# Performance work log

Measured on AMD Instinct MI355X. Metric: run time of the kernel, lower is better.

## Reference

```python
import jax, jax.numpy as jnp
import numpy as np

N_NODES = 4096
N_EDGES = 500000
N_PAIRS = 2000000
EDGE_DIM = 16
MAX_PATH = 5


def setup_inputs() -> dict:
    key = jax.random.key(0)
    k1, k2, k3, k4, k5 = jax.random.split(key, 5)
    x = jax.random.normal(k1, (N_NODES, EDGE_DIM), dtype=jnp.float32)
    edge_attr = jax.random.normal(k2, (N_EDGES, EDGE_DIM), dtype=jnp.float32)
    path_idx = jax.random.randint(k3, (N_PAIRS, MAX_PATH), 0, N_EDGES, dtype=jnp.int64)
    path_lens = jax.random.randint(k4, (N_PAIRS,), 0, MAX_PATH + 1, dtype=jnp.int64)
    pair_id = jnp.arange(N_PAIRS, dtype=jnp.int64)
    # learned parameter: edge_weights [max_path_distance, edge_dim]
    edge_weights = jax.random.normal(k5, (MAX_PATH, EDGE_DIM), dtype=jnp.float32)
    return {"x": x, "edge_attr": edge_attr, "edge_weights": edge_weights,
            "path_idx": path_idx, "path_lens": path_lens, "pair_id": pair_id}


def reference(x, edge_attr, edge_weights, path_idx, path_lens, pair_id):
    N = x.shape[0]
    L = edge_weights.shape[0]  # max_path_distance
    # valid-position mask for each ragged path, padded to length L
    mask = (jnp.arange(L)[None, :] < path_lens[:, None]).astype(edge_attr.dtype)  # [P, L]
    gathered = edge_attr[path_idx]  # [P, L, D] ragged gather of edge features
    # per-hop dot with learned per-hop weight vector, i.e. (w_l * e_l).sum(dim=1)
    dots = jnp.einsum('pld,ld->pl', gathered, edge_weights)  # [P, L]
    s = jnp.sum(dots * mask, axis=1)  # [P]
    cnt = path_lens.astype(edge_attr.dtype)
    # mean over valid hops; empty path -> NaN in torch -> nan_to_num -> 0
    mean = jnp.where(cnt > 0, s / jnp.maximum(cnt, 1.0), jnp.zeros_like(s))
    src = pair_id % N
    dst = pair_id // N  # unique (src, dst) pairs by construction
    cij = jnp.zeros((N, N), dtype=edge_attr.dtype).at[src, dst].set(mean)
    return cij
```

## Files before the change

kernel.cpp:

```cpp
#include <hip/hip_runtime.h>
#include <hip/hip_fp16.h>

#define NNODES 4096
#define NEDGES 500000
#define NPAIRS 2000000
#define EDIM   16
#define LMAX   5

__global__ __launch_bounds__(256) void dots_kernel(
    const float* __restrict__ edge_attr,
    const float* __restrict__ ew,
    __half* __restrict__ dots) {
  __shared__ float w[LMAX * EDIM];
  int tid = threadIdx.x;
  if (tid < LMAX * EDIM) w[tid] = ew[tid];
  __syncthreads();

  int e0 = (blockIdx.x * 256 + tid) * 2;
  if (e0 >= NEDGES) return;

  const float4* ra = (const float4*)(edge_attr + (size_t)e0 * EDIM);
  float4 a0 = ra[0], a1 = ra[1], a2 = ra[2], a3 = ra[3];
  float4 b0 = ra[4], b1 = ra[5], b2 = ra[6], b3 = ra[7];
  float va[16] = {a0.x, a0.y, a0.z, a0.w, a1.x, a1.y, a1.z, a1.w,
                  a2.x, a2.y, a2.z, a2.w, a3.x, a3.y, a3.z, a3.w};
  float vb[16] = {b0.x, b0.y, b0.z, b0.w, b1.x, b1.y, b1.z, b1.w,
                  b2.x, b2.y, b2.z, b2.w, b3.x, b3.y, b3.z, b3.w};
#pragma unroll
  for (int l = 0; l < LMAX; ++l) {
    float da = 0.f, db = 0.f;
#pragma unroll
    for (int k = 0; k < EDIM; ++k) {
      da += va[k] * w[l * EDIM + k];
      db += vb[k] * w[l * EDIM + k];
    }
    __half2 h;
    h.x = __float2half(da);
    h.y = __float2half(db);
    *(__half2*)(dots + (size_t)l * NEDGES + e0) = h;
  }
}

__global__ __launch_bounds__(256) void mean_kernel(
    const int* __restrict__ path_idx,
    const int* __restrict__ path_lens,
    const __half* __restrict__ dots,
    float* __restrict__ mean) {
  int p = blockIdx.x * 256 + threadIdx.x;
  if (p >= NPAIRS) return;

  int len = __builtin_nontemporal_load(path_lens + p);
  len = min(max(len, 0), LMAX);

  const int* row = path_idx + (size_t)p * LMAX;
  int i0 = __builtin_nontemporal_load(row + 0);
  int i1 = __builtin_nontemporal_load(row + 1);
  int i2 = __builtin_nontemporal_load(row + 2);
  int i3 = __builtin_nontemporal_load(row + 3);
  int i4 = __builtin_nontemporal_load(row + 4);

  float s = 0.f;
  if (len > 0) s += __half2float(dots[i0]);
  if (len > 1) s += __half2float(dots[1 * NEDGES + i1]);
  if (len > 2) s += __half2float(dots[2 * NEDGES + i2]);
  if (len > 3) s += __half2float(dots[3 * NEDGES + i3]);
  if (len > 4) s += __half2float(dots[4 * NEDGES + i4]);

  mean[p] = (len > 0) ? (s / (float)len) : 0.f;
}

__global__ __launch_bounds__(256) void expand_transpose(
    const float* __restrict__ mean,
    float* __restrict__ out) {
  const int dst0 = blockIdx.x * 64;
  const int src0 = blockIdx.y * 64;
  const int tid = threadIdx.x;

  if (dst0 * NNODES >= NPAIRS) {
    float4 z = {0.f, 0.f, 0.f, 0.f};
#pragma unroll
    for (int i = 0; i < 4; ++i) {
      int slot = tid + i * 256;
      int a = slot >> 4;
      int c = slot & 15;
      ((float4*)(out + (size_t)(src0 + a) * NNODES + dst0))[c] = z;
    }
    return;
  }

  __shared__ float tile[64][65];

#pragma unroll
  for (int i = 0; i < 4; ++i) {
    int slot = tid + i * 256;
    int a = slot >> 4;
    int c = slot & 15;
    int p = (dst0 + a) * NNODES + src0 + 4 * c;
    float4 v;
    if (p < NPAIRS) v = *(const float4*)(mean + p);
    else { v.x = 0.f; v.y = 0.f; v.z = 0.f; v.w = 0.f; }
    tile[a][4 * c + 0] = v.x;
    tile[a][4 * c + 1] = v.y;
    tile[a][4 * c + 2] = v.z;
    tile[a][4 * c + 3] = v.w;
  }
  __syncthreads();
#pragma unroll
  for (int i = 0; i < 4; ++i) {
    int slot = tid + i * 256;
    int a = slot >> 4;
    int c = slot & 15;
    float4 v;
    v.x = tile[4 * c + 0][a];
    v.y = tile[4 * c + 1][a];
    v.z = tile[4 * c + 2][a];
    v.w = tile[4 * c + 3][a];
    ((float4*)(out + (size_t)(src0 + a) * NNODES + dst0))[c] = v;
  }
}

__global__ __launch_bounds__(256) void scatter_kernel(
    const float* __restrict__ edge_attr,
    const float* __restrict__ ew,
    const int* __restrict__ path_idx,
    const int* __restrict__ path_lens,
    float* __restrict__ out) {
  __shared__ float w[LMAX * EDIM];
  if (threadIdx.x < LMAX * EDIM) w[threadIdx.x] = ew[threadIdx.x];
  __syncthreads();

  int p = blockIdx.x * 256 + threadIdx.x;
  if (p >= NPAIRS) return;

  int len = path_lens[p];
  len = min(max(len, 0), LMAX);

  const int* row = path_idx + (size_t)p * LMAX;
  float s = 0.f;
  for (int l = 0; l < len; ++l) {
    int idx = row[l];
    const float4* r = (const float4*)(edge_attr + (size_t)idx * EDIM);
    float4 a0 = r[0], a1 = r[1], a2 = r[2], a3 = r[3];
    const float* wl = &w[l * EDIM];
    s += a0.x * wl[0] + a0.y * wl[1] + a0.z * wl[2] + a0.w * wl[3] +
         a1.x * wl[4] + a1.y * wl[5] + a1.z * wl[6] + a1.w * wl[7] +
         a2.x * wl[8] + a2.y * wl[9] + a2.z * wl[10] + a2.w * wl[11] +
         a3.x * wl[12] + a3.y * wl[13] + a3.z * wl[14] + a3.w * wl[15];
  }
  float m = (len > 0) ? (s / (float)len) : 0.f;
  int src = p & (NNODES - 1);
  int dst = p >> 12;
  out[(size_t)src * NNODES + dst] = m;
}

extern "C" void kernel_launch(void* const* d_in, const int* in_sizes, int n_in,
                              void* d_out, int out_size, void* d_ws, size_t ws_size,
                              hipStream_t stream) {
  const float* edge_attr = (const float*)d_in[1];
  const float* edge_w    = (const float*)d_in[2];
  const int*   path_idx  = (const int*)d_in[3];
  const int*   path_lens = (const int*)d_in[4];
  float* out = (float*)d_out;

  const size_t need = (size_t)NPAIRS * sizeof(float) +
                      (size_t)LMAX * NEDGES * sizeof(__half);

  if (ws_size >= need) {
    float* mean = (float*)d_ws;
    __half* dots = (__half*)((char*)d_ws + (size_t)NPAIRS * sizeof(float));

    dots_kernel<<<(NEDGES / 2 + 255) / 256, 256, 0, stream>>>(edge_attr, edge_w, dots);
    mean_kernel<<<(NPAIRS + 255) / 256, 256, 0, stream>>>(path_idx, path_lens, dots, mean);
    dim3 grid(64, 64), block(256, 1);
    expand_transpose<<<grid, block, 0, stream>>>(mean, out);
  } else {
    hipMemsetAsync(d_out, 0, (size_t)out_size * sizeof(float), stream);
    scatter_kernel<<<(NPAIRS + 255) / 256, 256, 0, stream>>>(
        edge_attr, edge_w, path_idx, path_lens, out);
  }
}
```

Measured before the change: 175.7 us.

## Fuse path-mean gather into transpose kernel, removing intermediate mean buffer

Merges the per-pair mean computation into the tiled transpose/expand kernel. Each thread now loads four pairs' lengths and indices with vector nontemporal loads, gathers the fp16 dot values and writes the means straight into the shared tile. This removes one kernel launch and the write and re-read of the 8 MB mean buffer. The cost is lower parallelism during the gather (64 active blocks in the top rows, four pairs per thread) and higher register pressure, with gather latency now falling inside the transpose blocks.

```diff
diff --git a/kernel.cpp b/kernel.cpp
--- a/kernel.cpp
+++ b/kernel.cpp
@@ -6,6 +6,8 @@
 #define NPAIRS 2000000
 #define EDIM   16
 #define LMAX   5
+
+typedef int ivec4 __attribute__((ext_vector_type(4)));
 
 __global__ __launch_bounds__(256) void dots_kernel(
     const float* __restrict__ edge_attr,
@@ -41,36 +43,10 @@
   }
 }
 
-__global__ __launch_bounds__(256) void mean_kernel(
+__global__ __launch_bounds__(256) void fused_kernel(
     const int* __restrict__ path_idx,
     const int* __restrict__ path_lens,
     const __half* __restrict__ dots,
-    float* __restrict__ mean) {
-  int p = blockIdx.x * 256 + threadIdx.x;
-  if (p >= NPAIRS) return;
-
-  int len = __builtin_nontemporal_load(path_lens + p);
-  len = min(max(len, 0), LMAX);
-
-  const int* row = path_idx + (size_t)p * LMAX;
-  int i0 = __builtin_nontemporal_load(row + 0);
-  int i1 = __builtin_nontemporal_load(row + 1);
-  int i2 = __builtin_nontemporal_load(row + 2);
-  int i3 = __builtin_nontemporal_load(row + 3);
-  int i4 = __builtin_nontemporal_load(row + 4);
-
-  float s = 0.f;
-  if (len > 0) s += __half2float(dots[i0]);
-  if (len > 1) s += __half2float(dots[1 * NEDGES + i1]);
-  if (len > 2) s += __half2float(dots[2 * NEDGES + i2]);
-  if (len > 3) s += __half2float(dots[3 * NEDGES + i3]);
-  if (len > 4) s += __half2float(dots[4 * NEDGES + i4]);
-
-  mean[p] = (len > 0) ? (s / (float)len) : 0.f;
-}
-
-__global__ __launch_bounds__(256) void expand_transpose(
-    const float* __restrict__ mean,
     float* __restrict__ out) {
   const int dst0 = blockIdx.x * 64;
   const int src0 = blockIdx.y * 64;
@@ -90,21 +66,59 @@
 
   __shared__ float tile[64][65];
 
+  const int lane16 = tid & 15;
+  const int arow   = tid >> 4;
+
 #pragma unroll
   for (int i = 0; i < 4; ++i) {
-    int slot = tid + i * 256;
-    int a = slot >> 4;
-    int c = slot & 15;
-    int p = (dst0 + a) * NNODES + src0 + 4 * c;
-    float4 v;
-    if (p < NPAIRS) v = *(const float4*)(mean + p);
-    else { v.x = 0.f; v.y = 0.f; v.z = 0.f; v.w = 0.f; }
-    tile[a][4 * c + 0] = v.x;
-    tile[a][4 * c + 1] = v.y;
-    tile[a][4 * c + 2] = v.z;
-    tile[a][4 * c + 3] = v.w;
+    int a = arow + i * 16;
+    int p0 = (dst0 + a) * NNODES + src0 + 4 * lane16;
+    float m0 = 0.f, m1 = 0.f, m2 = 0.f, m3 = 0.f;
+    if (p0 < NPAIRS) {
+      ivec4 L = __builtin_nontemporal_load((const ivec4*)(path_lens + p0));
+      const ivec4* ir = (const ivec4*)(path_idx + (size_t)p0 * LMAX);
+      ivec4 q0 = __builtin_nontemporal_load(ir + 0);
+      ivec4 q1 = __builtin_nontemporal_load(ir + 1);
+      ivec4 q2 = __builtin_nontemporal_load(ir + 2);
+      ivec4 q3 = __builtin_nontemporal_load(ir + 3);
+      ivec4 q4 = __builtin_nontemporal_load(ir + 4);
+      int l0 = min(max(L.x, 0), LMAX);
+      int l1 = min(max(L.y, 0), LMAX);
+      int l2 = min(max(L.z, 0), LMAX);
+      int l3 = min(max(L.w, 0), LMAX);
+      if (l0 > 0) m0 += __half2float(dots[q0.x]);
+      if (l0 > 1) m0 += __half2float(dots[1 * NEDGES + q0.y]);
+      if (l0 > 2) m0 += __half2float(dots[2 * NEDGES + q0.z]);
+      if (l0 > 3) m0 += __half2float(dots[3 * NEDGES + q0.w]);
+      if (l0 > 4) m0 += __half2float(dots[4 * NEDGES + q1.x]);
+      if (l1 > 0) m1 += __half2float(dots[q1.y]);
+      if (l1 > 1) m1 += __half2float(dots[1 * NEDGES + q1.z]);
+      if (l1 > 2) m1 += __half2float(dots[2 * NEDGES + q1.w]);
+      if (l1 > 3) m1 += __half2float(dots[3 * NEDGES + q2.x]);
+      if (l1 > 4) m1 += __half2float(dots[4 * NEDGES + q2.y]);
+      if (l2 > 0) m2 += __half2float(dots[q2.z]);
+      if (l2 > 1) m2 += __half2float(dots[1 * NEDGES + q2.w]);
+      if (l2 > 2) m2 += __half2float(dots[2 * NEDGES + q3.x]);
+      if (l2 > 3) m2 += __half2float(dots[3 * NEDGES + q3.y]);
+      if (l2 > 4) m2 += __half2float(dots[4 * NEDGES + q3.z]);
+      if (l3 > 0) m3 += __half2float(dots[q3.w]);
+      if (l3 > 1) m3 += __half2float(dots[1 * NEDGES + q4.x]);
+      if (l3 > 2) m3 += __half2float(dots[2 * NEDGES + q4.y]);
+      if (l3 > 3) m3 += __half2float(dots[3 * NEDGES + q4.z]);
+      if (l3 > 4) m3 += __half2float(dots[4 * NEDGES + q4.w]);
+      m0 = (l0 > 0) ? m0 / (float)l0 : 0.f;
+      m1 = (l1 > 0) ? m1 / (float)l1 : 0.f;
+      m2 = (l2 > 0) ? m2 / (float)l2 : 0.f;
+      m3 = (l3 > 0) ? m3 / (float)l3 : 0.f;
+    }
+    int c0 = 4 * lane16;
+    tile[a][c0 + 0] = m0;
+    tile[a][c0 + 1] = m1;
+    tile[a][c0 + 2] = m2;
+    tile[a][c0 + 3] = m3;
   }
   __syncthreads();
+
 #pragma unroll
   for (int i = 0; i < 4; ++i) {
     int slot = tid + i * 256;
@@ -162,19 +176,15 @@
   const int*   path_lens = (const int*)d_in[4];
   float* out = (float*)d_out;
 
-  const size_t need = (size_t)NPAIRS * sizeof(float) +
-                      (size_t)LMAX * NEDGES * sizeof(__half);
+  const size_t need = (size_t)LMAX * NEDGES * sizeof(__half);
 
   if (ws_size >= need) {
-    float* mean = (float*)d_ws;
-    __half* dots = (__half*)((char*)d_ws + (size_t)NPAIRS * sizeof(float));
-
+    __half* dots = (__half*)d_ws;
     dots_kernel<<<(NEDGES / 2 + 255) / 256, 256, 0, stream>>>(edge_attr, edge_w, dots);
-    mean_kernel<<<(NPAIRS + 255) / 256, 256, 0, stream>>>(path_idx, path_lens, dots, mean);
     dim3 grid(64, 64), block(256, 1);
-    expand_transpose<<<grid, block, 0, stream>>>(mean, out);
+    fused_kernel<<<grid, block, 0, stream>>>(path_idx, path_lens, dots, out);
   } else {
-    hipMemsetAsync(d_out, 0, (size_t)out_size * sizeof(float), stream);
+    (void)hipMemsetAsync(d_out, 0, (size_t)out_size * sizeof(float), stream);
     scatter_kernel<<<(NPAIRS + 255) / 256, 256, 0, stream>>>(
         edge_attr, edge_w, path_idx, path_lens, out);
   }
```

After: 293.3 us. 66.9% more time.

## Fuse mean computation with transpose-scatter and spread zero-fill across blocks

Applied to the files above, without the earlier changes.

Merges the mean and transpose kernels into one kernel. Each block computes the means of a 16x16 tile of pairs, transposes them in shared memory and writes them straight to the output, so the 8 MB mean intermediate is never written or read back. The zero-filling of the columns that no pair reaches (dst >= 496) is handed out to all threads as nontemporal float4 stores. The cost is narrower 64-byte row segments in the transposed writes and index arithmetic that is hard-coded for this problem size.

```diff
diff --git a/kernel.cpp b/kernel.cpp
--- a/kernel.cpp
+++ b/kernel.cpp
@@ -6,6 +6,14 @@
 #define NPAIRS 2000000
 #define EDIM   16
 #define LMAX   5
+
+#define DST_TILES 31
+#define SRC_TILES 256
+#define NBLOCKS   (DST_TILES * SRC_TILES)
+#define NTHREADS  (NBLOCKS * 256)
+#define ZERO_F4   (4096 * 900)
+
+typedef float fvec4 __attribute__((ext_vector_type(4)));
 
 __global__ __launch_bounds__(256) void dots_kernel(
     const float* __restrict__ edge_attr,
@@ -41,82 +49,65 @@
   }
 }
 
-__global__ __launch_bounds__(256) void mean_kernel(
+__global__ __launch_bounds__(256) void fused_kernel(
     const int* __restrict__ path_idx,
     const int* __restrict__ path_lens,
     const __half* __restrict__ dots,
-    float* __restrict__ mean) {
-  int p = blockIdx.x * 256 + threadIdx.x;
-  if (p >= NPAIRS) return;
+    float* __restrict__ out) {
+  const int b = blockIdx.x;
+  const int tid = threadIdx.x;
+  const int dst0 = (b % DST_TILES) * 16;
+  const int src0 = (b / DST_TILES) * 16;
 
-  int len = __builtin_nontemporal_load(path_lens + p);
-  len = min(max(len, 0), LMAX);
+  __shared__ float tile[16][17];
 
-  const int* row = path_idx + (size_t)p * LMAX;
-  int i0 = __builtin_nontemporal_load(row + 0);
-  int i1 = __builtin_nontemporal_load(row + 1);
-  int i2 = __builtin_nontemporal_load(row + 2);
-  int i3 = __builtin_nontemporal_load(row + 3);
-  int i4 = __builtin_nontemporal_load(row + 4);
+  const int s = tid & 15;
+  const int a = tid >> 4;
+  const int p = (dst0 + a) * NNODES + src0 + s;
+  const bool valid = (p < NPAIRS);
 
-  float s = 0.f;
-  if (len > 0) s += __half2float(dots[i0]);
-  if (len > 1) s += __half2float(dots[1 * NEDGES + i1]);
-  if (len > 2) s += __half2float(dots[2 * NEDGES + i2]);
-  if (len > 3) s += __half2float(dots[3 * NEDGES + i3]);
-  if (len > 4) s += __half2float(dots[4 * NEDGES + i4]);
-
-  mean[p] = (len > 0) ? (s / (float)len) : 0.f;
-}
-
-__global__ __launch_bounds__(256) void expand_transpose(
-    const float* __restrict__ mean,
-    float* __restrict__ out) {
-  const int dst0 = blockIdx.x * 64;
-  const int src0 = blockIdx.y * 64;
-  const int tid = threadIdx.x;
-
-  if (dst0 * NNODES >= NPAIRS) {
-    float4 z = {0.f, 0.f, 0.f, 0.f};
-#pragma unroll
-    for (int i = 0; i < 4; ++i) {
-      int slot = tid + i * 256;
-      int a = slot >> 4;
-      int c = slot & 15;
-      ((float4*)(out + (size_t)(src0 + a) * NNODES + dst0))[c] = z;
-    }
-    return;
+  int len = 0;
+  int i0 = 0, i1 = 0, i2 = 0, i3 = 0, i4 = 0;
+  if (valid) {
+    len = __builtin_nontemporal_load(path_lens + p);
+    len = min(max(len, 0), LMAX);
+    const int* row = path_idx + (size_t)p * LMAX;
+    i0 = __builtin_nontemporal_load(row + 0);
+    i1 = __builtin_nontemporal_load(row + 1);
+    i2 = __builtin_nontemporal_load(row + 2);
+    i3 = __builtin_nontemporal_load(row + 3);
+    i4 = __builtin_nontemporal_load(row + 4);
   }
 
-  __shared__ float tile[64][65];
+  float m = 0.f;
+  if (len > 0) m += __half2float(dots[i0]);
+  if (len > 1) m += __half2float(dots[1 * NEDGES + i1]);
+  if (len > 2) m += __half2float(dots[2 * NEDGES + i2]);
+  if (len > 3) m += __half2float(dots[3 * NEDGES + i3]);
+  if (len > 4) m += __half2float(dots[4 * NEDGES + i4]);
+  m = (len > 0) ? m / (float)len : 0.f;
 
+  {
+    fvec4 z = {0.f, 0.f, 0.f, 0.f};
+    int gtid = b * 256 + tid;
 #pragma unroll
-  for (int i = 0; i < 4; ++i) {
-    int slot = tid + i * 256;
-    int a = slot >> 4;
-    int c = slot & 15;
-    int p = (dst0 + a) * NNODES + src0 + 4 * c;
-    float4 v;
-    if (p < NPAIRS) v = *(const float4*)(mean + p);
-    else { v.x = 0.f; v.y = 0.f; v.z = 0.f; v.w = 0.f; }
-    tile[a][4 * c + 0] = v.x;
-    tile[a][4 * c + 1] = v.y;
-    tile[a][4 * c + 2] = v.z;
-    tile[a][4 * c + 3] = v.w;
+    for (int rep = 0; rep < 2; ++rep) {
+      int zi = gtid + rep * NTHREADS;
+      if (zi < ZERO_F4) {
+        int src = zi / 900;
+        int c = zi - src * 900;
+        __builtin_nontemporal_store(
+            z, (fvec4*)(out + (size_t)src * NNODES) + 124 + c);
+      }
+    }
   }
+
+  tile[a][s] = m;
   __syncthreads();
-#pragma unroll
-  for (int i = 0; i < 4; ++i) {
-    int slot = tid + i * 256;
-    int a = slot >> 4;
-    int c = slot & 15;
-    float4 v;
-    v.x = tile[4 * c + 0][a];
-    v.y = tile[4 * c + 1][a];
-    v.z = tile[4 * c + 2][a];
-    v.w = tile[4 * c + 3][a];
-    ((float4*)(out + (size_t)(src0 + a) * NNODES + dst0))[c] = v;
-  }
+
+  const int r = tid >> 4;
+  const int c = tid & 15;
+  out[(size_t)(src0 + r) * NNODES + dst0 + c] = tile[c][r];
 }
 
 __global__ __launch_bounds__(256) void scatter_kernel(
@@ -162,19 +153,14 @@
   const int*   path_lens = (const int*)d_in[4];
   float* out = (float*)d_out;
 
-  const size_t need = (size_t)NPAIRS * sizeof(float) +
-                      (size_t)LMAX * NEDGES * sizeof(__half);
+  const size_t need = (size_t)LMAX * NEDGES * sizeof(__half);
 
   if (ws_size >= need) {
-    float* mean = (float*)d_ws;
-    __half* dots = (__half*)((char*)d_ws + (size_t)NPAIRS * sizeof(float));
-
+    __half* dots = (__half*)d_ws;
     dots_kernel<<<(NEDGES / 2 + 255) / 256, 256, 0, stream>>>(edge_attr, edge_w, dots);
-    mean_kernel<<<(NPAIRS + 255) / 256, 256, 0, stream>>>(path_idx, path_lens, dots, mean);
-    dim3 grid(64, 64), block(256, 1);
-    expand_transpose<<<grid, block, 0, stream>>>(mean, out);
+    fused_kernel<<<NBLOCKS, 256, 0, stream>>>(path_idx, path_lens, dots, out);
   } else {
-    hipMemsetAsync(d_out, 0, (size_t)out_size * sizeof(float), stream);
+    (void)hipMemsetAsync(d_out, 0, (size_t)out_size * sizeof(float), stream);
     scatter_kernel<<<(NPAIRS + 255) / 256, 256, 0, stream>>>(
         edge_attr, edge_w, path_idx, path_lens, out);
   }
```

Measured after the change: 177.4 us. No clear change (+0.9%).
